# Optimization experiments

Hardware: AMD Instinct MI355X
Metric: run time of the kernel (lower is better)

Reference implementation:

```python
import jax, jax.numpy as jnp
import numpy as np

B, T, NB = 8192, 18, 6
EH, DH = 256, 256
NIN = NB + 1  # encoder GRU input: bits + feedback scalar


def gru_cell(x, h, Wih, Whh, bih, bhh):
    # PyTorch GRU cell: gates ordered (r, z, n)
    gi = x @ Wih.T + bih
    gh = h @ Whh.T + bhh
    ir, iz, inn = jnp.split(gi, 3, axis=-1)
    hr, hz, hn = jnp.split(gh, 3, axis=-1)
    r = jax.nn.sigmoid(ir + hr)
    z = jax.nn.sigmoid(iz + hz)
    n = jnp.tanh(inn + r * hn)
    return (1.0 - z) * n + z * h


def run_gru_dir(seq, Wih, Whh, bih, bhh, reverse):
    # seq: [T, B, D] -> hidden outputs [T, B, H] (aligned to original time order)
    Bn, H = seq.shape[1], Whh.shape[1]
    def step(h, x):
        h2 = gru_cell(x, h, Wih, Whh, bih, bhh)
        return h2, h2
    _, outs = jax.lax.scan(step, jnp.zeros((Bn, H), seq.dtype), seq, reverse=reverse)
    return outs


def setup_inputs() -> dict:
    key = jax.random.key(0)
    ks = jax.random.split(key, 40)
    def w(k, shape, fan):
        s = 1.0 / np.sqrt(fan)
        return jax.random.uniform(k, shape, jnp.float32, -s, s)
    inp = {}
    inp['b'] = (jax.random.uniform(ks[0], (B, NB)) < 0.5).astype(jnp.float32)
    inp['noise1'] = jax.random.normal(ks[1], (B, T, 1), jnp.float32)
    inp['noise2'] = jax.random.normal(ks[2], (B, T, 1), jnp.float32)
    # encoder GRU (2 layers, unidirectional)
    inp['enc_Wih0'] = w(ks[3], (3 * EH, NIN), EH); inp['enc_Whh0'] = w(ks[4], (3 * EH, EH), EH)
    inp['enc_bih0'] = w(ks[5], (3 * EH,), EH);     inp['enc_bhh0'] = w(ks[6], (3 * EH,), EH)
    inp['enc_Wih1'] = w(ks[7], (3 * EH, EH), EH);  inp['enc_Whh1'] = w(ks[8], (3 * EH, EH), EH)
    inp['enc_bih1'] = w(ks[9], (3 * EH,), EH);     inp['enc_bhh1'] = w(ks[10], (3 * EH,), EH)
    inp['enc_lin_W'] = w(ks[11], (1, EH), EH);     inp['enc_lin_b'] = w(ks[12], (1,), EH)
    inp['weight_power'] = jnp.ones((T,), jnp.float32)
    # decoder GRU (2 layers, bidirectional)
    inp['dec_Wih0f'] = w(ks[13], (3 * DH, 1), DH);      inp['dec_Whh0f'] = w(ks[14], (3 * DH, DH), DH)
    inp['dec_bih0f'] = w(ks[15], (3 * DH,), DH);        inp['dec_bhh0f'] = w(ks[16], (3 * DH,), DH)
    inp['dec_Wih0b'] = w(ks[17], (3 * DH, 1), DH);      inp['dec_Whh0b'] = w(ks[18], (3 * DH, DH), DH)
    inp['dec_bih0b'] = w(ks[19], (3 * DH,), DH);        inp['dec_bhh0b'] = w(ks[20], (3 * DH,), DH)
    inp['dec_Wih1f'] = w(ks[21], (3 * DH, 2 * DH), DH); inp['dec_Whh1f'] = w(ks[22], (3 * DH, DH), DH)
    inp['dec_bih1f'] = w(ks[23], (3 * DH,), DH);        inp['dec_bhh1f'] = w(ks[24], (3 * DH,), DH)
    inp['dec_Wih1b'] = w(ks[25], (3 * DH, 2 * DH), DH); inp['dec_Whh1b'] = w(ks[26], (3 * DH, DH), DH)
    inp['dec_bih1b'] = w(ks[27], (3 * DH,), DH);        inp['dec_bhh1b'] = w(ks[28], (3 * DH,), DH)
    inp['dec_lin_W'] = w(ks[29], (NB, 2 * DH), 2 * DH); inp['dec_lin_b'] = w(ks[30], (NB,), 2 * DH)
    inp['weight_merge'] = jnp.ones((T, 2), jnp.float32)
    return inp


def reference(b, noise1, noise2,
              enc_Wih0, enc_Whh0, enc_bih0, enc_bhh0,
              enc_Wih1, enc_Whh1, enc_bih1, enc_bhh1,
              enc_lin_W, enc_lin_b, weight_power,
              dec_Wih0f, dec_Whh0f, dec_bih0f, dec_bhh0f,
              dec_Wih0b, dec_Whh0b, dec_bih0b, dec_bhh0b,
              dec_Wih1f, dec_Whh1f, dec_bih1f, dec_bhh1f,
              dec_Wih1b, dec_Whh1b, dec_bih1b, dec_bhh1b,
              dec_lin_W, dec_lin_b, weight_merge):
    Bn = b.shape[0]
    Tn = weight_power.shape[0]
    # power-normalized per-step weights: sqrt(w^2 * T / sum(w^2))
    wp = jnp.sqrt(weight_power ** 2 * Tn / jnp.sum(weight_power ** 2))

    def enc_step(carry, xs):
        h0, h1, z = carry
        n1, n2, wpt = xs
        inp = jnp.concatenate([b, z], axis=1)            # [B, NB+1]
        h0n = gru_cell(inp, h0, enc_Wih0, enc_Whh0, enc_bih0, enc_bhh0)
        h1n = gru_cell(h0n, h1, enc_Wih1, enc_Whh1, enc_bih1, enc_bhh1)
        xt = jnp.tanh(h1n @ enc_lin_W.T + enc_lin_b)     # [B, 1]
        xn = (xt - jnp.mean(xt)) / jnp.std(xt, ddof=1)   # training-mode batch norm over whole tensor
        y = xn * wpt + n1                                # received symbol
        return (h0n, h1n, y + n2), y                     # feedback z = y + noise2

    carry0 = (jnp.zeros((Bn, EH), b.dtype), jnp.zeros((Bn, EH), b.dtype), jnp.zeros((Bn, 1), b.dtype))
    xs = (jnp.swapaxes(noise1, 0, 1), jnp.swapaxes(noise2, 0, 1), wp)
    _, y_seq = jax.lax.scan(enc_step, carry0, xs)        # [T, B, 1]

    # bidirectional 2-layer decoder GRU over y
    o0f = run_gru_dir(y_seq, dec_Wih0f, dec_Whh0f, dec_bih0f, dec_bhh0f, False)
    o0b = run_gru_dir(y_seq, dec_Wih0b, dec_Whh0b, dec_bih0b, dec_bhh0b, True)
    s1 = jnp.concatenate([o0f, o0b], axis=-1)            # [T, B, 2*DH]
    o1f = run_gru_dir(s1, dec_Wih1f, dec_Whh1f, dec_bih1f, dec_bhh1f, False)
    o1b = run_gru_dir(s1, dec_Wih1b, dec_Whh1b, dec_bih1b, dec_bhh1b, True)

    # attention_type == 5: learned weighted merge over time, per direction
    wf = jnp.sqrt(weight_merge[:, 0] ** 2 * Tn / jnp.sum(weight_merge[:, 0] ** 2))
    wb = jnp.sqrt(weight_merge[:, 1] ** 2 * Tn / jnp.sum(weight_merge[:, 1] ** 2))
    rf = jnp.einsum('tbh,t->bh', o1f, wf)
    rb = jnp.einsum('tbh,t->bh', o1b, wb)
    rc = jnp.concatenate([rf, rb], axis=1)               # [B, 2*DH]
    out = jax.nn.sigmoid(rc @ dec_lin_W.T + dec_lin_b)   # bit_vector output -> sigmoid
    return out.reshape(Bn, -1, 1)
```

## Files before the change

### kernel.cpp

```cpp
#include <hip/hip_runtime.h>
#include <hip/hip_bf16.h>
#include <math.h>

#define BN_ 8192
#define TT 18
#define NBITS 6
#define HH 256
#define G3 768

typedef __hip_bfloat16 hbf16;
typedef __bf16 bf16x8 __attribute__((ext_vector_type(8)));
typedef float f32x4 __attribute__((ext_vector_type(4)));

__device__ inline float sigm(float x){ return 1.0f/(1.0f + expf(-x)); }
__device__ inline float ldx(const void* p, int i, int bf){
    if(bf){ unsigned short u = ((const unsigned short*)p)[i]; return __uint_as_float(((unsigned)u)<<16); }
    return ((const float*)p)[i];
}
__device__ inline __bf16 f2b(float f){ hbf16 h = __float2bfloat16(f); return *reinterpret_cast<__bf16*>(&h); }
__device__ inline float b2f(__bf16 b){ unsigned short u = *reinterpret_cast<unsigned short*>(&b); return __uint_as_float(((unsigned)u)<<16); }
__device__ inline unsigned pack2(float a, float b){
    hbf16 lo = __float2bfloat16(a), hi = __float2bfloat16(b);
    return (unsigned)*(unsigned short*)&lo | ((unsigned)*(unsigned short*)&hi << 16);
}

__device__ __forceinline__ void gld_lds16(const void* g, void* l){
    __builtin_amdgcn_global_load_lds(
        (const __attribute__((address_space(1))) unsigned int*)g,
        (__attribute__((address_space(3))) unsigned int*)l, 16, 0, 0);
}

__global__ __launch_bounds__(256) void fillz(float* __restrict__ p, int n){
    for(int i = blockIdx.x*256 + threadIdx.x; i < n; i += gridDim.x*256) p[i] = 0.0f;
}
__global__ __launch_bounds__(256) void fillb(__bf16* __restrict__ p, int n){
    for(int i = blockIdx.x*256 + threadIdx.x; i < n; i += gridDim.x*256) p[i] = f2b(0.0f);
}

__global__ void prep_w(const void* wp, const void* wm, unsigned* flag,
                       float* wpn, float* wfn, float* wbn){
    if(threadIdx.x==0 && blockIdx.x==0){
        unsigned w0 = *(const unsigned*)wp;
        int bf = ((w0 >> 16) == (w0 & 0xFFFFu)) ? 1 : 0;
        flag[0] = (unsigned)bf;
        float s=0; for(int t=0;t<TT;t++){ float v=ldx(wp,t,bf); s += v*v; }
        for(int t=0;t<TT;t++){ float v=ldx(wp,t,bf); wpn[t] = sqrtf(v*v*TT/s); }
        float sf=0, sb=0;
        for(int t=0;t<TT;t++){ float f=ldx(wm,2*t,bf), b=ldx(wm,2*t+1,bf); sf += f*f; sb += b*b; }
        for(int t=0;t<TT;t++){
            float f=ldx(wm,2*t,bf), b=ldx(wm,2*t+1,bf);
            wfn[t] = sqrtf(f*f*TT/sf);
            wbn[t] = sqrtf(b*b*TT/sb);
        }
    }
}

struct CJ { const void* src; void* dst; int n; int K; int mode; };
struct CJs { CJ j[20]; };
__global__ __launch_bounds__(256) void conv_all(CJs J, const unsigned* __restrict__ flagp){
    const int bf = (int)*flagp;
    CJ c = J.j[blockIdx.y];
    for(int i = blockIdx.x*256 + threadIdx.x; i < c.n; i += gridDim.x*256){
        if(c.mode==1){
            int row = i / c.K, k = i - row*c.K;
            int g = row>>8, jj = row&255;
            int prow = ((jj>>4)*48) + g*16 + (jj&15);
            ((__bf16*)c.dst)[(size_t)prow*c.K + k] = f2b(ldx(c.src, i, bf));
        }else if(c.mode==2){
            int t = i >> 13, b = i & (BN_-1);
            ((float*)c.dst)[i] = ldx(c.src, b*TT + t, bf);
        }else{
            ((float*)c.dst)[i] = ldx(c.src, i, bf);
        }
    }
}

struct FQ {
    const __bf16* A1; const __bf16* W1; int K1;
    const __bf16* A2; const __bf16* W2; int K2;
    const float* bgi; const float* bgh;
    const __bf16* h; __bf16* hout;
    const void* bits; const void* wih0raw; const void* bih0raw;
    const void* linw; float* xt;
    const float* y; const void* wihraw; const void* bihraw; __bf16* s1t;
    float* racc; const float* wct;
};
struct FQ2 { FQ q[2]; };

template<int MODE>
__global__ __launch_bounds__(256,3) void fused_step(FQ2 PP, const unsigned* __restrict__ flagp){
    const FQ P = PP.q[blockIdx.z];
    const int bf = (int)*flagp;
    __shared__ __align__(16) char smem[28672];
    __shared__ float zs[192];
    __shared__ float sred[4], ssred[4];
    __bf16* As = (__bf16*)smem;
    __bf16* Ws = (__bf16*)(smem + 16384);
    float*  T  = (float*)smem;
    const int tid = threadIdx.x;
    const int mt = blockIdx.x*8 + (blockIdx.y>>3);
    const int jt = blockIdx.y & 7;
    const int m0 = mt*128;
    const int n0 = jt*96;
    const int lane = tid&63, wv = tid>>6;
    const int wvbase = tid & ~63;
    const int wrow = wv>>1, wcol = wv&1;
    const int q = lane>>4, n15 = lane&15;

    if(MODE==0){
        if(P.K1){
            const float lbv = ldx(P.linw, 0, bf);
            const float wt  = P.wct[0];
            const float* __restrict__ xr = P.xt;
            float s=0.0f, ss=0.0f;
            const float4* x4 = (const float4*)xr;
            for(int i=tid;i<BN_/4;i+=256){
                float4 vv = x4[i];
                float a0=tanhf(vv.x+lbv), a1=tanhf(vv.y+lbv), a2=tanhf(vv.z+lbv), a3=tanhf(vv.w+lbv);
                s += a0+a1+a2+a3; ss += a0*a0+a1*a1+a2*a2+a3*a3;
            }
            #pragma unroll
            for(int o=32;o;o>>=1){ s += __shfl_xor(s,o); ss += __shfl_xor(ss,o); }
            if(lane==0){ sred[wv]=s; ssred[wv]=ss; }
            __syncthreads();
            float a = sred[0]+sred[1]+sred[2]+sred[3];
            float bq = ssred[0]+ssred[1]+ssred[2]+ssred[3];
            float mean = a/(float)BN_;
            float var = (bq - (float)BN_*mean*mean)/(float)(BN_-1);
            float rs = 1.0f/sqrtf(var);
            if(tid<128){
                int row = m0 + tid;
                float v = tanhf(xr[row]+lbv);
                float yv = (v-mean)*rs*wt + P.y[row];
                zs[tid] = yv + ((const float*)P.wihraw)[row];
                if(jt==0){ ((float*)P.s1t)[row] = yv; P.racc[row] = 0.0f; }
            }
        }else{
            if(tid<128) zs[tid] = 0.0f;
        }
        __syncthreads();
    }

    f32x4 accR[4], accZ[4], accN1[4], accN2[4];
    #pragma unroll
    for(int i=0;i<4;i++){ accR[i]=(f32x4){0,0,0,0}; accZ[i]=(f32x4){0,0,0,0};
                          accN1[i]=(f32x4){0,0,0,0}; accN2[i]=(f32x4){0,0,0,0}; }

    #pragma unroll
    for(int ph = 0; ph < 2; ph++){
        if(ph==0 && !(MODE==1 || MODE==3)) continue;
        const __bf16* __restrict__ A = ph ? P.A2 : P.A1;
        const __bf16* __restrict__ W = ph ? P.W2 : P.W1;
        const int K = ph ? P.K2 : P.K1;
        for(int k0=0;k0<K;k0+=64){
            #pragma unroll
            for(int s=0;s<4;s++){
                int c = tid + 256*s;
                int row = c>>3, slot = c&7;
                int qc = slot ^ ((row>>1)&7);
                gld_lds16(A + (size_t)(m0+row)*K + k0 + qc*8,
                          smem + (s*256 + wvbase)*16);
            }
            #pragma unroll
            for(int s=0;s<3;s++){
                int c = tid + 256*s;
                int row = c>>3, slot = c&7;
                int qc = slot ^ ((row>>1)&7);
                gld_lds16(W + (size_t)(n0+row)*K + k0 + qc*8,
                          smem + 16384 + (s*256 + wvbase)*16);
            }
            __syncthreads();
            #pragma unroll
            for(int ks=0;ks<2;ks++){
                const int cq = ks*4 + q;
                bf16x8 af[4], bfr[3];
                #pragma unroll
                for(int i=0;i<4;i++){
                    int R = wrow*64+i*16+n15;
                    int col = cq ^ ((R>>1)&7);
                    af[i] = *(const bf16x8*)&As[R*64 + col*8];
                }
                #pragma unroll
                for(int g=0;g<3;g++){
                    int RW = wcol*48+g*16+n15;
                    int col = cq ^ ((RW>>1)&7);
                    bfr[g] = *(const bf16x8*)&Ws[RW*64 + col*8];
                }
                #pragma unroll
                for(int i=0;i<4;i++){
                    accR[i] = __builtin_amdgcn_mfma_f32_16x16x32_bf16(af[i], bfr[0], accR[i], 0,0,0);
                    accZ[i] = __builtin_amdgcn_mfma_f32_16x16x32_bf16(af[i], bfr[1], accZ[i], 0,0,0);
                    if(ph) accN2[i] = __builtin_amdgcn_mfma_f32_16x16x32_bf16(af[i], bfr[2], accN2[i], 0,0,0);
                    else   accN1[i] = __builtin_amdgcn_mfma_f32_16x16x32_bf16(af[i], bfr[2], accN1[i], 0,0,0);
                }
            }
            __syncthreads();
        }
    }

    const int jl = wcol*16 + n15;
    const int j  = jt*32 + jl;
    const float bghr = P.bgh[j], bghz = P.bgh[256+j], bghn = P.bgh[512+j];
    float bgir=0, bgiz=0, bgin=0;
    if(MODE==1 || MODE==3){ bgir = P.bgi[j]; bgiz = P.bgi[256+j]; bgin = P.bgi[512+j]; }
    float w0r[7], w0z[7], w0n[7];
    if(MODE==0){
        #pragma unroll
        for(int k=0;k<7;k++){
            w0r[k] = ldx(P.wih0raw, (j    )*7+k, bf);
            w0z[k] = ldx(P.wih0raw, (j+256)*7+k, bf);
            w0n[k] = ldx(P.wih0raw, (j+512)*7+k, bf);
        }
        bgir = ldx(P.bih0raw, j, bf); bgiz = ldx(P.bih0raw, j+256, bf); bgin = ldx(P.bih0raw, j+512, bf);
    }
    float wy_r=0, wy_z=0, wy_n=0;
    if(MODE==2){
        wy_r = ldx(P.wihraw, j, bf); wy_z = ldx(P.wihraw, j+256, bf); wy_n = ldx(P.wihraw, j+512, bf);
        bgir = ldx(P.bihraw, j, bf); bgiz = ldx(P.bihraw, j+256, bf); bgin = ldx(P.bihraw, j+512, bf);
    }
    const float linwj = (MODE==1) ? ldx(P.linw, j, bf) : 0.0f;

    #pragma unroll
    for(int i=0;i<4;i++){
        const int rbl = wrow*64 + i*16 + q*4;
        float vred[4];
        #pragma unroll
        for(int r=0;r<4;r++){
            const int row_l = rbl + r;
            const int row = m0 + row_l;
            float gir, giz, gin;
            if(MODE==1 || MODE==3){
                gir = bgir; giz = bgiz; gin = accN1[i][r] + bgin;
            }else if(MODE==0){
                gir = bgir; giz = bgiz; gin = bgin;
                #pragma unroll
                for(int k=0;k<NBITS;k++){
                    float bv = ldx(P.bits, row*NBITS+k, bf);
                    gir += bv*w0r[k]; giz += bv*w0z[k]; gin += bv*w0n[k];
                }
                float zb = zs[row_l];
                gir += zb*w0r[6]; giz += zb*w0z[6]; gin += zb*w0n[6];
            }else{
                float yv = P.y[row];
                gir = yv*wy_r + bgir; giz = yv*wy_z + bgiz; gin = yv*wy_n + bgin;
            }
            float rr = sigm(gir + accR[i][r] + bghr);
            float zz = sigm(giz + accZ[i][r] + bghz);
            float nn = tanhf(gin + rr*(accN2[i][r] + bghn));
            float hold = b2f(P.h[(size_t)row*HH + j]);
            float hn = (1.0f - zz)*nn + zz*hold;
            T[row_l*33 + jl] = hn;
            if(MODE==1) vred[r] = hn*linwj;
        }
        if(MODE==1){
            #pragma unroll
            for(int r=0;r<4;r++){
                float v = vred[r];
                #pragma unroll
                for(int m=1;m<16;m<<=1) v += __shfl_xor(v, m);
                if(n15==0) atomicAdd(&P.xt[m0+rbl+r], v);
            }
        }
    }
    if(MODE==3 && tid<192){
        int k = tid>>5, jj = tid&31;
        zs[tid] = ldx(P.bits, k*512 + (int)blockIdx.z*256 + jt*32 + jj, bf);
    }
    __syncthreads();

    const int rw2 = tid>>2, cw = tid&3;
    #pragma unroll
    for(int pass=0; pass<2; pass++){
        const int row_l = pass*64 + rw2;
        const int row = m0 + row_l;
        float v[8];
        #pragma unroll
        for(int u=0;u<8;u++) v[u] = T[row_l*33 + cw*8 + u];
        uint4 pkv = { pack2(v[0],v[1]), pack2(v[2],v[3]), pack2(v[4],v[5]), pack2(v[6],v[7]) };
        *(uint4*)&P.hout[(size_t)row*HH + jt*32 + cw*8] = pkv;
        if(MODE==2) *(uint4*)&P.s1t[(size_t)row*512 + jt*32 + cw*8] = pkv;
    }
    if(MODE==3){
        float* pp = P.xt + (size_t)(jt + 8*(int)blockIdx.z)*(BN_*NBITS);
        const float wct3 = P.wct[0];
        #pragma unroll
        for(int u=0;u<3;u++){
            int idx = tid + 256*u;
            int row_l = idx/6, k = idx - row_l*6;
            float dot = 0.0f;
            #pragma unroll
            for(int jj=0;jj<32;jj++) dot += T[row_l*33+jj]*zs[k*32+jj];
            size_t gi = (size_t)(m0+row_l)*NBITS + k;
            pp[gi] += wct3*dot;
        }
    }
}

__global__ __launch_bounds__(1024) void stats_emit(float* __restrict__ xt, const void* __restrict__ lb,
        const float* __restrict__ wpn, int t, const float* __restrict__ n1t, const float* __restrict__ n2t,
        float* __restrict__ yseq, float* __restrict__ zf, const unsigned* __restrict__ flagp){
    const int bf = (int)*flagp;
    const float lbv = ldx(lb, 0, bf);
    int tid = threadIdx.x;
    float s=0.0f, ss=0.0f;
    for(int i=tid;i<BN_;i+=1024){ float v = tanhf(xt[i] + lbv); s += v; ss += v*v; }
    #pragma unroll
    for(int o=32;o;o>>=1){ s += __shfl_down(s,o); ss += __shfl_down(ss,o); }
    __shared__ float S[16], SS[16], stm[2];
    if((tid&63)==0){ S[tid>>6]=s; SS[tid>>6]=ss; }
    __syncthreads();
    if(tid==0){
        float a=0.0f, b=0.0f;
        for(int i=0;i<16;i++){ a+=S[i]; b+=SS[i]; }
        float mean = a/(float)BN_;
        float var = (b - (float)BN_*mean*mean)/(float)(BN_-1);
        stm[0]=mean; stm[1]=1.0f/sqrtf(var);
    }
    __syncthreads();
    const float mean=stm[0], rs=stm[1], wt=wpn[t];
    for(int i=tid;i<BN_;i+=1024){
        float v = tanhf(xt[i] + lbv);
        float y = (v-mean)*rs*wt + n1t[i];
        yseq[(size_t)t*BN_ + i] = y;
        zf[i] = y + n2t[i];
        xt[i] = 0.0f;
    }
}

__global__ __launch_bounds__(256) void out_head(const float* __restrict__ pp, const void* __restrict__ bias,
        void* __restrict__ out, const unsigned* __restrict__ flagp){
    const int bf = (int)*flagp;
    int i = blockIdx.x*256 + threadIdx.x;
    if(i >= BN_*NBITS) return;
    float s = 0.0f;
    #pragma unroll
    for(int k=0;k<16;k++) s += pp[(size_t)k*(BN_*NBITS) + i];
    int kk = i - (i/6)*6;
    float v = sigm(s + ldx(bias, kk, bf));
    if(bf) ((hbf16*)out)[i] = __float2bfloat16(v);
    else   ((float*)out)[i] = v;
}

extern "C" void kernel_launch(void* const* d_in, const int* in_sizes, int n_in,
                              void* d_out, int out_size, void* d_ws, size_t ws_size,
                              hipStream_t stream)
{
    (void)in_sizes; (void)n_in; (void)out_size;
    const void* bits  = d_in[0];
    const void* n1    = d_in[1];
    const void* n2    = d_in[2];
    const void* eWih0 = d_in[3];
    const void* eWhh0 = d_in[4];
    const void* ebih0 = d_in[5];
    const void* ebhh0 = d_in[6];
    const void* eWih1 = d_in[7];
    const void* eWhh1 = d_in[8];
    const void* ebih1 = d_in[9];
    const void* ebhh1 = d_in[10];
    const void* elinW = d_in[11];
    const void* elinb = d_in[12];
    const void* wpow  = d_in[13];
    const void* dWih0f= d_in[14];
    const void* dWhh0f= d_in[15];
    const void* dbih0f= d_in[16];
    const void* dbhh0f= d_in[17];
    const void* dWih0b= d_in[18];
    const void* dWhh0b= d_in[19];
    const void* dbih0b= d_in[20];
    const void* dbhh0b= d_in[21];
    const void* dWih1f= d_in[22];
    const void* dWhh1f= d_in[23];
    const void* dbih1f= d_in[24];
    const void* dbhh1f= d_in[25];
    const void* dWih1b= d_in[26];
    const void* dWhh1b= d_in[27];
    const void* dbih1b= d_in[28];
    const void* dbhh1b= d_in[29];
    const void* dlinW = d_in[30];
    const void* dlinb = d_in[31];
    const void* wmrg  = d_in[32];

    float* base = (float*)d_ws;
    size_t off = 0;
    auto alloc  = [&](size_t n){ float* p = base + off; off += (n + 63) & ~(size_t)63; return p; };
    auto allocb = [&](size_t n){ __bf16* p = (__bf16*)(base + off); off += ((n/2) + 63) & ~(size_t)63; return p; };
    unsigned* flag = (unsigned*)alloc(64);
    float* wpn = alloc(TT); float* wfn = alloc(TT); float* wbn = alloc(TT);
    const int WK = HH*G3;
    __bf16* WeHH0 = allocb(WK);  __bf16* WeIH1 = allocb(WK);  __bf16* WeHH1 = allocb(WK);
    __bf16* Wd0f  = allocb(WK);  __bf16* Wd0b  = allocb(WK);
    __bf16* Wd1fI = allocb(2*WK);__bf16* Wd1bI = allocb(2*WK);
    __bf16* Wd1fH = allocb(WK);  __bf16* Wd1bH = allocb(WK);
    float* BeHH0 = alloc(G3); float* BeIH1 = alloc(G3); float* BeHH1 = alloc(G3);
    float* Bd0f  = alloc(G3); float* Bd0b  = alloc(G3);
    float* Bd1fI = alloc(G3); float* Bd1bI = alloc(G3);
    float* Bd1fH = alloc(G3); float* Bd1bH = alloc(G3);
    const size_t NH = (size_t)BN_*HH;
    __bf16* X0 = allocb(NH);  __bf16* X1 = allocb(NH);
    __bf16* Y0 = allocb(NH);  __bf16* Y1 = allocb(NH);
    float* pout = alloc((size_t)16*BN_*NBITS);
    float* xtA = alloc(BN_);
    float* xtB = alloc(BN_);
    float* zf  = alloc(BN_);
    float* yseq= alloc((size_t)TT*BN_);
    float* n1t = alloc((size_t)TT*BN_);
    float* n2t = alloc((size_t)TT*BN_);
    __bf16* s1 = allocb((size_t)TT*BN_*512);
    size_t need = off*sizeof(float);
    if(ws_size < need) return;

    prep_w<<<1,64,0,stream>>>(wpow, wmrg, flag, wpn, wfn, wbn);
    CJs J;
    const void* ws_src[20] = {eWhh0,eWih1,eWhh1,dWhh0f,dWhh0b,dWih1f,dWih1b,dWhh1f,dWhh1b,
                              ebhh0,ebih1,ebhh1,dbhh0f,dbhh0b,dbih1f,dbih1b,dbhh1f,dbhh1b, n1, n2};
    void* ws_dst[20] = {WeHH0,WeIH1,WeHH1,Wd0f,Wd0b,Wd1fI,Wd1bI,Wd1fH,Wd1bH,
                        BeHH0,BeIH1,BeHH1,Bd0f,Bd0b,Bd1fI,Bd1bI,Bd1fH,Bd1bH, n1t, n2t};
    int ws_n[20] = {WK,WK,WK,WK,WK,2*WK,2*WK,WK,WK, G3,G3,G3,G3,G3,G3,G3,G3,G3, TT*BN_, TT*BN_};
    int ws_K[20] = {256,256,256,256,256,512,512,256,256, 0,0,0,0,0,0,0,0,0, 0,0};
    int ws_m[20] = {1,1,1,1,1,1,1,1,1, 0,0,0,0,0,0,0,0,0, 2,2};
    for(int i=0;i<20;i++){ J.j[i] = {ws_src[i], ws_dst[i], ws_n[i], ws_K[i], ws_m[i]}; }
    conv_all<<<dim3(768,20),256,0,stream>>>(J, flag);
    fillb<<<1024,256,0,stream>>>(X0, (int)NH);
    fillb<<<1024,256,0,stream>>>(Y0, (int)NH);
    fillz<<<32,256,0,stream>>>(xtA, BN_);
    fillz<<<32,256,0,stream>>>(xtB, BN_);
    fillz<<<192,256,0,stream>>>(pout, 16*BN_*NBITS);

    dim3 g1(8, 64, 1), g2(8, 64, 2);
    __bf16* X[2] = {X0, X1};
    __bf16* Y[2] = {Y0, Y1};
    float* xts[2] = {xtA, xtB};

    int p = 0;
    for(int t=0;t<TT;t++){
        FQ2 P0{}; FQ2 P1{};
        FQ& a = P0.q[0];
        a.A2=X[p]; a.W2=WeHH0; a.K2=HH; a.bgh=BeHH0; a.h=X[p]; a.hout=X[1-p];
        a.bits=bits; a.wih0raw=eWih0; a.bih0raw=ebih0;
        a.K1 = (t>0) ? 1 : 0;
        if(t>0){
            a.xt   = xts[(t-1)&1];
            a.racc = xts[t&1];
            a.y    = n1t + (size_t)(t-1)*BN_;
            a.wihraw = (const void*)(n2t + (size_t)(t-1)*BN_);
            a.s1t  = (__bf16*)(yseq + (size_t)(t-1)*BN_);
            a.wct  = wpn + (t-1);
            a.linw = elinb;
        }
        fused_step<0><<<g1,256,0,stream>>>(P0, flag);
        FQ& b = P1.q[0];
        b.A1=X[1-p]; b.W1=WeIH1; b.K1=HH; b.A2=Y[p]; b.W2=WeHH1; b.K2=HH;
        b.bgi=BeIH1; b.bgh=BeHH1; b.h=Y[p]; b.hout=Y[1-p];
        b.linw=elinW; b.xt=xts[t&1];
        fused_step<1><<<g1,256,0,stream>>>(P1, flag);
        p ^= 1;
    }
    stats_emit<<<1,1024,0,stream>>>(xts[(TT-1)&1], elinb, wpn, TT-1,
                                    n1t+(size_t)(TT-1)*BN_, n2t+(size_t)(TT-1)*BN_, yseq, zf, flag);

    fillb<<<1024,256,0,stream>>>(X0, (int)NH);
    fillb<<<1024,256,0,stream>>>(Y0, (int)NH);
    p = 0;
    for(int i=0;i<TT;i++){
        int tf = i, tb = TT-1-i;
        FQ2 P{};
        FQ& a = P.q[0];
        a.A2=X[p]; a.W2=Wd0f; a.K2=HH; a.bgh=Bd0f; a.h=X[p]; a.hout=X[1-p];
        a.y=yseq+(size_t)tf*BN_; a.wihraw=dWih0f; a.bihraw=dbih0f; a.s1t=s1+(size_t)tf*BN_*512;
        FQ& b = P.q[1];
        b.A2=Y[p]; b.W2=Wd0b; b.K2=HH; b.bgh=Bd0b; b.h=Y[p]; b.hout=Y[1-p];
        b.y=yseq+(size_t)tb*BN_; b.wihraw=dWih0b; b.bihraw=dbih0b; b.s1t=s1+(size_t)tb*BN_*512+256;
        fused_step<2><<<g2,256,0,stream>>>(P, flag);
        p ^= 1;
    }

    fillb<<<1024,256,0,stream>>>(X0, (int)NH);
    fillb<<<1024,256,0,stream>>>(Y0, (int)NH);
    p = 0;
    for(int i=0;i<TT;i++){
        int tf = i, tb = TT-1-i;
        FQ2 P{};
        FQ& a = P.q[0];
        a.A1=s1+(size_t)tf*BN_*512; a.W1=Wd1fI; a.K1=512;
        a.A2=X[p]; a.W2=Wd1fH; a.K2=HH; a.bgi=Bd1fI; a.bgh=Bd1fH; a.h=X[p]; a.hout=X[1-p];
        a.bits=dlinW; a.xt=pout; a.wct=wfn+tf;
        FQ& b = P.q[1];
        b.A1=s1+(size_t)tb*BN_*512; b.W1=Wd1bI; b.K1=512;
        b.A2=Y[p]; b.W2=Wd1bH; b.K2=HH; b.bgi=Bd1bI; b.bgh=Bd1bH; b.h=Y[p]; b.hout=Y[1-p];
        b.bits=dlinW; b.xt=pout; b.wct=wbn+tb;
        fused_step<3><<<g2,256,0,stream>>>(P, flag);
        p ^= 1;
    }

    out_head<<<192,256,0,stream>>>(pout, dlinb, d_out, flag);
}
```

Measured before the change: 1.791 ms.

## Double-buffer GEMM K-loop with 32-wide stages and prefetch before prologue

Replaces the single-buffered 64-wide K loop with a double-buffered pipeline of 32-wide K stages, where the next stage's global-to-LDS copy is issued before the current stage's MFMAs run. The first stage is issued before the MODE 0 normalization prologue, so that load overlaps with it. K dimensions become compile-time constants per MODE, and the swizzle changes to match the narrower rows. This aims to hide global load latency and drop one barrier per iteration, at the cost of more iterations and hardcoded K sizes.

New measurement: 1.792 ms. No clear change (+0.0%).

```diff
diff --git a/kernel.cpp b/kernel.cpp
--- a/kernel.cpp
+++ b/kernel.cpp
@@ -94,8 +94,6 @@
     __shared__ __align__(16) char smem[28672];
     __shared__ float zs[192];
     __shared__ float sred[4], ssred[4];
-    __bf16* As = (__bf16*)smem;
-    __bf16* Ws = (__bf16*)(smem + 16384);
     float*  T  = (float*)smem;
     const int tid = threadIdx.x;
     const int mt = blockIdx.x*8 + (blockIdx.y>>3);
@@ -106,6 +104,33 @@
     const int wvbase = tid & ~63;
     const int wrow = wv>>1, wcol = wv&1;
     const int q = lane>>4, n15 = lane&15;
+
+    constexpr int S1  = (MODE==1) ? 8 : (MODE==3 ? 16 : 0);
+    constexpr int NST = S1 + 8;
+    constexpr int KD1 = (MODE==3) ? 512 : 256;
+    constexpr int KD2 = 256;
+    const __bf16* pA1 = (S1>0) ? P.A1 + (size_t)m0*KD1 : (const __bf16*)nullptr;
+    const __bf16* pW1 = (S1>0) ? P.W1 + (size_t)n0*KD1 : (const __bf16*)nullptr;
+    const __bf16* pA2 = P.A2 + (size_t)m0*KD2;
+    const __bf16* pW2 = P.W2 + (size_t)n0*KD2;
+    const int r0 = tid>>2, sl0 = tid&3;
+    const int q0 = sl0 ^ ((r0>>1)&3);
+    const int r1 = (256+tid)>>2, sl1 = tid&3;
+    const int q1 = sl1 ^ ((r1>>1)&3);
+
+    auto STG = [&](int s){
+        const __bf16* A; const __bf16* W; int K; int k0;
+        if(s < S1){ A = pA1; W = pW1; K = KD1; k0 = s*32; }
+        else      { A = pA2; W = pW2; K = KD2; k0 = (s-S1)*32; }
+        char* buf = smem + (s&1)*14336;
+        gld_lds16(A + (size_t)r0*K + k0 + q0*8, buf + (size_t)wvbase*16);
+        gld_lds16(A + (size_t)r1*K + k0 + q1*8, buf + (size_t)(256+wvbase)*16);
+        gld_lds16(W + (size_t)r0*K + k0 + q0*8, buf + 8192 + (size_t)wvbase*16);
+        if(tid < 128)
+            gld_lds16(W + (size_t)r1*K + k0 + q1*8, buf + 8192 + (size_t)(256+wvbase)*16);
+    };
+
+    STG(0);
 
     if(MODE==0){
         if(P.K1){
@@ -139,6 +164,8 @@
             if(tid<128) zs[tid] = 0.0f;
         }
         __syncthreads();
+    }else{
+        __syncthreads();
     }
 
     f32x4 accR[4], accZ[4], accN1[4], accN2[4];
@@ -147,55 +174,32 @@
                           accN1[i]=(f32x4){0,0,0,0}; accN2[i]=(f32x4){0,0,0,0}; }
 
     #pragma unroll
-    for(int ph = 0; ph < 2; ph++){
-        if(ph==0 && !(MODE==1 || MODE==3)) continue;
-        const __bf16* __restrict__ A = ph ? P.A2 : P.A1;
-        const __bf16* __restrict__ W = ph ? P.W2 : P.W1;
-        const int K = ph ? P.K2 : P.K1;
-        for(int k0=0;k0<K;k0+=64){
-            #pragma unroll
-            for(int s=0;s<4;s++){
-                int c = tid + 256*s;
-                int row = c>>3, slot = c&7;
-                int qc = slot ^ ((row>>1)&7);
-                gld_lds16(A + (size_t)(m0+row)*K + k0 + qc*8,
-                          smem + (s*256 + wvbase)*16);
-            }
-            #pragma unroll
-            for(int s=0;s<3;s++){
-                int c = tid + 256*s;
-                int row = c>>3, slot = c&7;
-                int qc = slot ^ ((row>>1)&7);
-                gld_lds16(W + (size_t)(n0+row)*K + k0 + qc*8,
-                          smem + 16384 + (s*256 + wvbase)*16);
-            }
-            __syncthreads();
-            #pragma unroll
-            for(int ks=0;ks<2;ks++){
-                const int cq = ks*4 + q;
-                bf16x8 af[4], bfr[3];
-                #pragma unroll
-                for(int i=0;i<4;i++){
-                    int R = wrow*64+i*16+n15;
-                    int col = cq ^ ((R>>1)&7);
-                    af[i] = *(const bf16x8*)&As[R*64 + col*8];
-                }
-                #pragma unroll
-                for(int g=0;g<3;g++){
-                    int RW = wcol*48+g*16+n15;
-                    int col = cq ^ ((RW>>1)&7);
-                    bfr[g] = *(const bf16x8*)&Ws[RW*64 + col*8];
-                }
-                #pragma unroll
-                for(int i=0;i<4;i++){
-                    accR[i] = __builtin_amdgcn_mfma_f32_16x16x32_bf16(af[i], bfr[0], accR[i], 0,0,0);
-                    accZ[i] = __builtin_amdgcn_mfma_f32_16x16x32_bf16(af[i], bfr[1], accZ[i], 0,0,0);
-                    if(ph) accN2[i] = __builtin_amdgcn_mfma_f32_16x16x32_bf16(af[i], bfr[2], accN2[i], 0,0,0);
-                    else   accN1[i] = __builtin_amdgcn_mfma_f32_16x16x32_bf16(af[i], bfr[2], accN1[i], 0,0,0);
-                }
-            }
-            __syncthreads();
-        }
+    for(int s=0; s<NST; ++s){
+        if(s+1 < NST) STG(s+1);
+        const char* buf = smem + (s&1)*14336;
+        const __bf16* Asb = (const __bf16*)buf;
+        const __bf16* Wsb = (const __bf16*)(buf + 8192);
+        bf16x8 af[4], bfr[3];
+        #pragma unroll
+        for(int i=0;i<4;i++){
+            int R = wrow*64+i*16+n15;
+            int col = q ^ ((R>>1)&3);
+            af[i] = *(const bf16x8*)&Asb[R*32 + col*8];
+        }
+        #pragma unroll
+        for(int g=0;g<3;g++){
+            int RW = wcol*48+g*16+n15;
+            int col = q ^ ((RW>>1)&3);
+            bfr[g] = *(const bf16x8*)&Wsb[RW*32 + col*8];
+        }
+        #pragma unroll
+        for(int i=0;i<4;i++){
+            accR[i] = __builtin_amdgcn_mfma_f32_16x16x32_bf16(af[i], bfr[0], accR[i], 0,0,0);
+            accZ[i] = __builtin_amdgcn_mfma_f32_16x16x32_bf16(af[i], bfr[1], accZ[i], 0,0,0);
+            if(s < S1) accN1[i] = __builtin_amdgcn_mfma_f32_16x16x32_bf16(af[i], bfr[2], accN1[i], 0,0,0);
+            else       accN2[i] = __builtin_amdgcn_mfma_f32_16x16x32_bf16(af[i], bfr[2], accN2[i], 0,0,0);
+        }
+        __syncthreads();
     }
 
     const int jl = wcol*16 + n15;
```
